# Kernel optimization log

Measured on AMD Instinct MI355X. Metric: run time of the kernel, lower is better.

The kernel has to match this reference:

```python
import jax, jax.numpy as jnp
import numpy as np

FP8_MAX = 448.0  # e4m3 max
SCALE_MARGIN = 0.8


def _fp8_quant_dequant(t, scale):
    # scaled value is <= 448*0.8 by construction, so no saturation/overflow
    q = (t / scale).astype(jnp.float8_e4m3fn)
    return q.astype(jnp.float32) * scale


def setup_inputs() -> dict:
    key = jax.random.key(0)
    k1, k2 = jax.random.split(key)
    B, S, D_IN, D_OUT = 4, 2048, 2048, 2048
    x = jax.random.normal(k1, (B, S, D_IN), dtype=jnp.float32)
    weight = jax.random.normal(k2, (D_OUT, D_IN), dtype=jnp.float32)
    bias = jnp.zeros((D_OUT,), dtype=jnp.float32)
    return {"x": x, "weight": weight, "bias": bias}


def reference(x, weight, bias):
    # Shared FP8ScalingManager: amax history = [amax_x] for x, then [amax_x, amax_w] for w.
    amax_x = jnp.max(jnp.abs(x))
    amax_w = jnp.max(jnp.abs(weight))
    x_scale = amax_x / (FP8_MAX * SCALE_MARGIN)
    w_scale = jnp.maximum(amax_x, amax_w) / (FP8_MAX * SCALE_MARGIN)  # history max
    x_scale = jax.lax.stop_gradient(x_scale)  # .item() detaches in torch
    w_scale = jax.lax.stop_gradient(w_scale)
    # quantize to fp8 e4m3, dequantize, scaled matmul (math of torch._scaled_mm)
    x_dq = _fp8_quant_dequant(x, x_scale)      # [B,S,Din]
    w_dq = _fp8_quant_dequant(weight, w_scale)  # [Dout,Din]
    out = jnp.einsum('bsd,od->bso', x_dq, w_dq)  # [B,S,Dout]
    return out + bias
```

## Files before the change

kernel.cpp:

```cpp
#include <hip/hip_runtime.h>
#include <stdint.h>

typedef float v4f __attribute__((ext_vector_type(4)));
typedef int v8i __attribute__((ext_vector_type(8)));

#define FP8_DENOM 358.4f


__device__ __forceinline__ unsigned pack4_fp8(float a, float b, float c, float d) {
  int v = 0;
  v = __builtin_amdgcn_cvt_pk_fp8_f32(a, b, v, false);
  v = __builtin_amdgcn_cvt_pk_fp8_f32(c, d, v, true);
  return (unsigned)v;
}

__device__ __forceinline__ void gload_lds16(const void* g, void* l) {
  __builtin_amdgcn_global_load_lds(
      (const __attribute__((address_space(1))) uint32_t*)(uintptr_t)g,
      (__attribute__((address_space(3))) uint32_t*)(uint32_t)(uintptr_t)l,
      16, 0, 0);
}


__global__ void __launch_bounds__(256) amax_part(const float4* __restrict__ x,
                                                 const float4* __restrict__ w,
                                                 float* __restrict__ part) {
  const int b = blockIdx.x, t = threadIdx.x;
  const float4* p = (b < 1024) ? x : w;
  const long base = (long)((b < 1024) ? b : (b - 1024)) * 4096;
  float m0 = 0.f, m1 = 0.f, m2 = 0.f, m3 = 0.f;
#pragma unroll
  for (int j = 0; j < 4; ++j) {
    float4 v0 = p[base + (j * 4 + 0) * 256 + t];
    float4 v1 = p[base + (j * 4 + 1) * 256 + t];
    float4 v2 = p[base + (j * 4 + 2) * 256 + t];
    float4 v3 = p[base + (j * 4 + 3) * 256 + t];
    m0 = fmaxf(m0, fmaxf(fmaxf(fabsf(v0.x), fabsf(v0.y)), fmaxf(fabsf(v0.z), fabsf(v0.w))));
    m1 = fmaxf(m1, fmaxf(fmaxf(fabsf(v1.x), fabsf(v1.y)), fmaxf(fabsf(v1.z), fabsf(v1.w))));
    m2 = fmaxf(m2, fmaxf(fmaxf(fabsf(v2.x), fabsf(v2.y)), fmaxf(fabsf(v2.z), fabsf(v2.w))));
    m3 = fmaxf(m3, fmaxf(fmaxf(fabsf(v3.x), fabsf(v3.y)), fmaxf(fabsf(v3.z), fabsf(v3.w))));
  }
  float m = fmaxf(fmaxf(m0, m1), fmaxf(m2, m3));
#pragma unroll
  for (int off = 32; off > 0; off >>= 1)
    m = fmaxf(m, __shfl_down(m, off, 64));
  __shared__ float red[4];
  const int lane = t & 63, wvid = t >> 6;
  if (lane == 0) red[wvid] = m;
  __syncthreads();
  if (t == 0) part[b] = fmaxf(fmaxf(red[0], red[1]), fmaxf(red[2], red[3]));
}


__global__ void __launch_bounds__(256) scale_reduce(const float* __restrict__ part,
                                                    unsigned* __restrict__ amax) {
  const int t = threadIdx.x;
  float mx = fmaxf(fmaxf(part[t], part[t + 256]), fmaxf(part[t + 512], part[t + 768]));
  float mw = part[1024 + t];
#pragma unroll
  for (int off = 32; off > 0; off >>= 1) {
    mx = fmaxf(mx, __shfl_down(mx, off, 64));
    mw = fmaxf(mw, __shfl_down(mw, off, 64));
  }
  __shared__ float rx[4], rw[4];
  const int lane = t & 63, wvid = t >> 6;
  if (lane == 0) { rx[wvid] = mx; rw[wvid] = mw; }
  __syncthreads();
  if (t == 0) {
    const float ax = fmaxf(fmaxf(rx[0], rx[1]), fmaxf(rx[2], rx[3]));
    const float aw = fmaxf(fmaxf(rw[0], rw[1]), fmaxf(rw[2], rw[3]));
    const float sx = ax / FP8_DENOM;
    const float sw = fmaxf(ax, aw) / FP8_DENOM;
    amax[0] = __float_as_uint(ax);
    amax[1] = __float_as_uint(aw);
    amax[2] = __float_as_uint(1.0f / sx);
    amax[3] = __float_as_uint(1.0f / sw);
    amax[4] = __float_as_uint(sx * sw);
  }
}


__global__ void quant2_kernel(const float4* __restrict__ x, uint4* __restrict__ xq, int nx16,
                              const float4* __restrict__ w, uint4* __restrict__ wq, int nw16,
                              int xblocks, const unsigned* __restrict__ amax) {
  const int isw = ((int)blockIdx.x >= xblocks) ? 1 : 0;
  const float rs = __uint_as_float(amax[2 + isw]);
  const float4* in = isw ? w : x;
  uint4* outq = isw ? wq : xq;
  const int n16 = isw ? nw16 : nx16;
  const int b0 = isw ? ((int)blockIdx.x - xblocks) : (int)blockIdx.x;
  const int nb = isw ? ((int)gridDim.x - xblocks) : xblocks;
  const long stride = (long)nb * blockDim.x;
  for (long i = (long)b0 * blockDim.x + threadIdx.x; i < n16; i += stride) {
    float4 v0 = in[4 * i + 0], v1 = in[4 * i + 1], v2 = in[4 * i + 2], v3 = in[4 * i + 3];
    uint4 r;
    r.x = pack4_fp8(v0.x * rs, v0.y * rs, v0.z * rs, v0.w * rs);
    r.y = pack4_fp8(v1.x * rs, v1.y * rs, v1.z * rs, v1.w * rs);
    r.z = pack4_fp8(v2.x * rs, v2.y * rs, v2.z * rs, v2.w * rs);
    r.w = pack4_fp8(v3.x * rs, v3.y * rs, v3.z * rs, v3.w * rs);
    outq[i] = r;
  }
}


__global__ void __launch_bounds__(256) gemm_mx(
    const uint8_t* __restrict__ Aq, const uint8_t* __restrict__ Bq,
    const float* __restrict__ bias, float* __restrict__ out,
    const unsigned* __restrict__ amax) {
  constexpr int K = 2048, N = 2048, BK = 128, ITERS = K / BK;
  __shared__ alignas(16) uint8_t sA[2][128 * BK];
  __shared__ alignas(16) uint8_t sB[2][128 * BK];

  const int tid = threadIdx.x;
  const int lane = tid & 63;
  const int wid = tid >> 6;
  const int wy = wid >> 1, wx = wid & 1;
  const long tileM = (long)blockIdx.y * 128;
  const long tileN = (long)blockIdx.x * 128;

  v4f acc[4][4];
#pragma unroll
  for (int i = 0; i < 4; ++i)
#pragma unroll
    for (int j = 0; j < 4; ++j) acc[i][j] = (v4f)(0.f);

  const int srow = tid >> 3;
  const int schunk = (tid & 7) ^ (srow & 7);
  const uint8_t* gA = Aq + (tileM + srow) * K + schunk * 16;
  const uint8_t* gB = Bq + (tileN + srow) * K + schunk * 16;

  const int q = lane >> 4;
  const int mrow = lane & 15;

  int aoff[4][2], boff[4][2];
#pragma unroll
  for (int i = 0; i < 4; ++i) {
    const int rA = wy * 64 + i * 16 + mrow, swA = rA & 7;
    aoff[i][0] = rA * 128 + 16 * ((2 * q) ^ swA);
    aoff[i][1] = rA * 128 + 16 * ((2 * q + 1) ^ swA);
    const int rB = wx * 64 + i * 16 + mrow, swB = rB & 7;
    boff[i][0] = rB * 128 + 16 * ((2 * q) ^ swB);
    boff[i][1] = rB * 128 + 16 * ((2 * q + 1) ^ swB);
  }

  auto stage = [&](int buf, int k0) {
#pragma unroll
    for (int s = 0; s < 4; ++s) {
      gload_lds16(gA + (long)s * 32 * K + k0, &sA[buf][s * 4096 + tid * 16]);
      gload_lds16(gB + (long)s * 32 * K + k0, &sB[buf][s * 4096 + tid * 16]);
    }
  };

  stage(0, 0);
  for (int it = 0; it < ITERS; ++it) {
    __syncthreads();
    if (it + 1 < ITERS) stage((it + 1) & 1, (it + 1) * BK);

    const uint8_t* bufA = sA[it & 1];
    const uint8_t* bufB = sB[it & 1];
    union Frag { v8i v; uint4 h[2]; };
    Frag a[4], b[4];
#pragma unroll
    for (int i = 0; i < 4; ++i) {
      a[i].h[0] = *(const uint4*)(bufA + aoff[i][0]);
      a[i].h[1] = *(const uint4*)(bufA + aoff[i][1]);
      b[i].h[0] = *(const uint4*)(bufB + boff[i][0]);
      b[i].h[1] = *(const uint4*)(bufB + boff[i][1]);
    }
#pragma unroll
    for (int i = 0; i < 4; ++i)
#pragma unroll
      for (int j = 0; j < 4; ++j)
        acc[i][j] = __builtin_amdgcn_mfma_scale_f32_16x16x128_f8f6f4(
            a[i].v, b[j].v, acc[i][j],  0,  0,
             0, 0x7F7F7F7F,  0, 0x7F7F7F7F);
  }

  const float scale = __uint_as_float(amax[4]);
#pragma unroll
  for (int j = 0; j < 4; ++j) {
    const long col = tileN + wx * 64 + j * 16 + mrow;
    const float bv = bias[col];
#pragma unroll
    for (int i = 0; i < 4; ++i) {
      const long row = tileM + wy * 64 + i * 16 + q * 4;
#pragma unroll
      for (int r = 0; r < 4; ++r)
        out[(row + r) * N + col] = acc[i][j][r] * scale + bv;
    }
  }
}


extern "C" void kernel_launch(void* const* d_in, const int* in_sizes, int n_in,
                              void* d_out, int out_size, void* d_ws, size_t ws_size,
                              hipStream_t stream) {
  const float* x = (const float*)d_in[0];
  const float* w = (const float*)d_in[1];
  const float* bias = (const float*)d_in[2];
  float* out = (float*)d_out;

  const int M = 8192, N = 2048, K = 2048;
  const long nx = (long)M * K, nw = (long)N * K;

  unsigned* amax = (unsigned*)d_ws;
  float* part = (float*)((uint8_t*)d_ws + 256);
  uint8_t* xq = (uint8_t*)d_ws + 8192;
  uint8_t* wq = xq + nx;

  amax_part<<<1280, 256, 0, stream>>>((const float4*)x, (const float4*)w, part);
  scale_reduce<<<1, 256, 0, stream>>>(part, amax);
  quant2_kernel<<<5120, 256, 0, stream>>>((const float4*)x, (uint4*)xq, (int)(nx / 16),
                                          (const float4*)w, (uint4*)wq, (int)(nw / 16),
                                          4096, amax);
  gemm_mx<<<dim3(N / 128, M / 128), 256, 0, stream>>>(xq, wq, bias, out, amax);
}
```

Measured before the change: 176.5 us.

## Enlarge GEMM tile to 256x256 with 8 waves and simplify quant kernel

The FP8 MFMA GEMM block tile grows from 128x128 to 256x256 with 512 threads. Each wave now computes 64x128 outputs, and B fragments are loaded in two halves to limit register use. This raises data reuse per LDS and global byte and shrinks the grid to 256 blocks, but doubles the LDS footprint to 128KB and uses more accumulator registers, which limits occupancy. The quantization kernel also drops its grid-stride loop for a fixed one-block-per-4096-elements mapping, with coalesced 4-byte stores.

```diff
diff --git a/kernel.cpp b/kernel.cpp
--- a/kernel.cpp
+++ b/kernel.cpp
@@ -80,49 +80,47 @@
 }
 
 
-__global__ void quant2_kernel(const float4* __restrict__ x, uint4* __restrict__ xq, int nx16,
-                              const float4* __restrict__ w, uint4* __restrict__ wq, int nw16,
-                              int xblocks, const unsigned* __restrict__ amax) {
-  const int isw = ((int)blockIdx.x >= xblocks) ? 1 : 0;
+__global__ void __launch_bounds__(256) quant_kernel(
+    const float4* __restrict__ x, unsigned* __restrict__ xq,
+    const float4* __restrict__ w, unsigned* __restrict__ wq,
+    const unsigned* __restrict__ amax) {
+  const int b = blockIdx.x, t = threadIdx.x;
+  const int isw = (b >= 4096) ? 1 : 0;
   const float rs = __uint_as_float(amax[2 + isw]);
   const float4* in = isw ? w : x;
-  uint4* outq = isw ? wq : xq;
-  const int n16 = isw ? nw16 : nx16;
-  const int b0 = isw ? ((int)blockIdx.x - xblocks) : (int)blockIdx.x;
-  const int nb = isw ? ((int)gridDim.x - xblocks) : xblocks;
-  const long stride = (long)nb * blockDim.x;
-  for (long i = (long)b0 * blockDim.x + threadIdx.x; i < n16; i += stride) {
-    float4 v0 = in[4 * i + 0], v1 = in[4 * i + 1], v2 = in[4 * i + 2], v3 = in[4 * i + 3];
-    uint4 r;
-    r.x = pack4_fp8(v0.x * rs, v0.y * rs, v0.z * rs, v0.w * rs);
-    r.y = pack4_fp8(v1.x * rs, v1.y * rs, v1.z * rs, v1.w * rs);
-    r.z = pack4_fp8(v2.x * rs, v2.y * rs, v2.z * rs, v2.w * rs);
-    r.w = pack4_fp8(v3.x * rs, v3.y * rs, v3.z * rs, v3.w * rs);
-    outq[i] = r;
-  }
-}
-
-
-__global__ void __launch_bounds__(256) gemm_mx(
+  unsigned* outq = isw ? wq : xq;
+  const long base = (long)(isw ? (b - 4096) : b) * 1024;
+  float4 v0 = in[base + 0 * 256 + t];
+  float4 v1 = in[base + 1 * 256 + t];
+  float4 v2 = in[base + 2 * 256 + t];
+  float4 v3 = in[base + 3 * 256 + t];
+  outq[base + 0 * 256 + t] = pack4_fp8(v0.x * rs, v0.y * rs, v0.z * rs, v0.w * rs);
+  outq[base + 1 * 256 + t] = pack4_fp8(v1.x * rs, v1.y * rs, v1.z * rs, v1.w * rs);
+  outq[base + 2 * 256 + t] = pack4_fp8(v2.x * rs, v2.y * rs, v2.z * rs, v2.w * rs);
+  outq[base + 3 * 256 + t] = pack4_fp8(v3.x * rs, v3.y * rs, v3.z * rs, v3.w * rs);
+}
+
+
+__global__ void __launch_bounds__(512, 2) gemm_mx(
     const uint8_t* __restrict__ Aq, const uint8_t* __restrict__ Bq,
     const float* __restrict__ bias, float* __restrict__ out,
     const unsigned* __restrict__ amax) {
   constexpr int K = 2048, N = 2048, BK = 128, ITERS = K / BK;
-  __shared__ alignas(16) uint8_t sA[2][128 * BK];
-  __shared__ alignas(16) uint8_t sB[2][128 * BK];
+  __shared__ alignas(16) uint8_t sA[2][256 * 128];
+  __shared__ alignas(16) uint8_t sB[2][256 * 128];
 
   const int tid = threadIdx.x;
   const int lane = tid & 63;
   const int wid = tid >> 6;
   const int wy = wid >> 1, wx = wid & 1;
-  const long tileM = (long)blockIdx.y * 128;
-  const long tileN = (long)blockIdx.x * 128;
-
-  v4f acc[4][4];
+  const long tileM = (long)blockIdx.y * 256;
+  const long tileN = (long)blockIdx.x * 256;
+
+  v4f acc[4][8];
 #pragma unroll
   for (int i = 0; i < 4; ++i)
 #pragma unroll
-    for (int j = 0; j < 4; ++j) acc[i][j] = (v4f)(0.f);
+    for (int j = 0; j < 8; ++j) acc[i][j] = (v4f)(0.f);
 
   const int srow = tid >> 3;
   const int schunk = (tid & 7) ^ (srow & 7);
@@ -132,24 +130,30 @@
   const int q = lane >> 4;
   const int mrow = lane & 15;
 
-  int aoff[4][2], boff[4][2];
+  int aoff[4][2], boff[8][2];
 #pragma unroll
   for (int i = 0; i < 4; ++i) {
     const int rA = wy * 64 + i * 16 + mrow, swA = rA & 7;
     aoff[i][0] = rA * 128 + 16 * ((2 * q) ^ swA);
     aoff[i][1] = rA * 128 + 16 * ((2 * q + 1) ^ swA);
-    const int rB = wx * 64 + i * 16 + mrow, swB = rB & 7;
-    boff[i][0] = rB * 128 + 16 * ((2 * q) ^ swB);
-    boff[i][1] = rB * 128 + 16 * ((2 * q + 1) ^ swB);
+  }
+#pragma unroll
+  for (int j = 0; j < 8; ++j) {
+    const int rB = wx * 128 + j * 16 + mrow, swB = rB & 7;
+    boff[j][0] = rB * 128 + 16 * ((2 * q) ^ swB);
+    boff[j][1] = rB * 128 + 16 * ((2 * q + 1) ^ swB);
   }
 
   auto stage = [&](int buf, int k0) {
 #pragma unroll
-    for (int s = 0; s < 4; ++s) {
-      gload_lds16(gA + (long)s * 32 * K + k0, &sA[buf][s * 4096 + tid * 16]);
-      gload_lds16(gB + (long)s * 32 * K + k0, &sB[buf][s * 4096 + tid * 16]);
-    }
+    for (int s = 0; s < 4; ++s)
+      gload_lds16(gA + (long)s * 64 * K + k0, &sA[buf][s * 8192 + tid * 16]);
+#pragma unroll
+    for (int s = 0; s < 4; ++s)
+      gload_lds16(gB + (long)s * 64 * K + k0, &sB[buf][s * 8192 + tid * 16]);
   };
+
+  union Frag { v8i v; uint4 h[2]; };
 
   stage(0, 0);
   for (int it = 0; it < ITERS; ++it) {
@@ -158,28 +162,34 @@
 
     const uint8_t* bufA = sA[it & 1];
     const uint8_t* bufB = sB[it & 1];
-    union Frag { v8i v; uint4 h[2]; };
-    Frag a[4], b[4];
+    Frag a[4];
 #pragma unroll
     for (int i = 0; i < 4; ++i) {
       a[i].h[0] = *(const uint4*)(bufA + aoff[i][0]);
       a[i].h[1] = *(const uint4*)(bufA + aoff[i][1]);
-      b[i].h[0] = *(const uint4*)(bufB + boff[i][0]);
-      b[i].h[1] = *(const uint4*)(bufB + boff[i][1]);
     }
 #pragma unroll
-    for (int i = 0; i < 4; ++i)
-#pragma unroll
-      for (int j = 0; j < 4; ++j)
-        acc[i][j] = __builtin_amdgcn_mfma_scale_f32_16x16x128_f8f6f4(
-            a[i].v, b[j].v, acc[i][j],  0,  0,
-             0, 0x7F7F7F7F,  0, 0x7F7F7F7F);
+    for (int jh = 0; jh < 2; ++jh) {
+      Frag bfr[4];
+#pragma unroll
+      for (int jj = 0; jj < 4; ++jj) {
+        bfr[jj].h[0] = *(const uint4*)(bufB + boff[jh * 4 + jj][0]);
+        bfr[jj].h[1] = *(const uint4*)(bufB + boff[jh * 4 + jj][1]);
+      }
+#pragma unroll
+      for (int i = 0; i < 4; ++i)
+#pragma unroll
+        for (int jj = 0; jj < 4; ++jj)
+          acc[i][jh * 4 + jj] = __builtin_amdgcn_mfma_scale_f32_16x16x128_f8f6f4(
+              a[i].v, bfr[jj].v, acc[i][jh * 4 + jj],  0,  0,
+               0, 0x7F7F7F7F,  0, 0x7F7F7F7F);
+    }
   }
 
   const float scale = __uint_as_float(amax[4]);
 #pragma unroll
-  for (int j = 0; j < 4; ++j) {
-    const long col = tileN + wx * 64 + j * 16 + mrow;
+  for (int j = 0; j < 8; ++j) {
+    const long col = tileN + wx * 128 + j * 16 + mrow;
     const float bv = bias[col];
 #pragma unroll
     for (int i = 0; i < 4; ++i) {
@@ -210,8 +220,7 @@
 
   amax_part<<<1280, 256, 0, stream>>>((const float4*)x, (const float4*)w, part);
   scale_reduce<<<1, 256, 0, stream>>>(part, amax);
-  quant2_kernel<<<5120, 256, 0, stream>>>((const float4*)x, (uint4*)xq, (int)(nx / 16),
-                                          (const float4*)w, (uint4*)wq, (int)(nw / 16),
-                                          4096, amax);
-  gemm_mx<<<dim3(N / 128, M / 128), 256, 0, stream>>>(xq, wq, bias, out, amax);
-}
+  quant_kernel<<<5120, 256, 0, stream>>>((const float4*)x, (unsigned*)xq,
+                                         (const float4*)w, (unsigned*)wq, amax);
+  gemm_mx<<<dim3(N / 256, M / 256), 512, 0, stream>>>(xq, wq, bias, out, amax);
+}
```

Result: no change. 177.4 us (+0.5%).
